# Optimization experiments

Hardware: AMD Instinct MI355X
Metric: run time of the kernel (lower is better)

The kernel has to match this reference:

```python
import jax, jax.numpy as jnp
import numpy as np

RADII = (0.8, 1.6)
NSAMPLES = (16, 32)
NUM_GRIDPOINTS = 216


def rotate_z(points, theta):
    # points (b, n, m, 3), theta (b, n); rotate xy about z-axis
    c = jnp.cos(theta)[:, :, None]
    s = jnp.sin(theta)[:, :, None]
    x, y, z = points[..., 0], points[..., 1], points[..., 2]
    return jnp.stack([c * x - s * y, s * x + c * y, z], axis=-1)


def ball_query(d2, radius, nsample):
    # d2: (b, Ng, K) squared distances. Returns first nsample in-radius point
    # indices per query (CUDA ball_query semantics: pad with first found index,
    # 0 if none found).
    K = d2.shape[-1]
    ar = jnp.arange(K, dtype=jnp.int32)
    scores = jnp.where(d2 < radius * radius, ar, K)  # K == sentinel for 'not in ball'
    idx = -jax.lax.top_k(-scores, nsample)[0]        # nsample smallest => first hits, ascending
    first = idx[..., :1]
    idx = jnp.where(idx >= K, first, idx)
    idx = jnp.where(idx >= K, 0, idx)
    return idx


def gather_group(xyz, feats_t, new_xyz, idx):
    # xyz (b,K,3), feats_t (b,K,C), new_xyz (b,Ng,3), idx (b,Ng,ns)
    gx = jax.vmap(lambda p, i: p[i])(xyz, idx)      # (b,Ng,ns,3)
    gf = jax.vmap(lambda f, i: f[i])(feats_t, idx)  # (b,Ng,ns,C)
    rel = gx - new_xyz[:, :, None, :]               # use_xyz=True relative coords
    return jnp.concatenate([rel, gf], axis=-1)      # (b,Ng,ns,3+C)


def setup_inputs() -> dict:
    key = jax.random.key(0)
    ks = jax.random.split(key, 12)
    b, n, m, K, C = 2, 48, NUM_GRIDPOINTS, 2048, 128
    proposals = jax.random.uniform(ks[0], (b, n, 7), dtype=jnp.float32)
    keypoint_xyz = jax.random.normal(ks[1], (b, K, 3), dtype=jnp.float32)
    keypoint_features = jax.random.normal(ks[2], (b, C, K), dtype=jnp.float32)
    grid_noise = jax.random.uniform(ks[3], (b, n, m, 3), dtype=jnp.float32)

    def lin(k, o, i):
        return jax.random.normal(k, (o, i), dtype=jnp.float32) / np.float32(np.sqrt(i))

    w0_0 = lin(ks[4], 64, C + 3)
    w0_1 = lin(ks[5], 64, 64)
    w1_0 = lin(ks[6], 64, C + 3)
    w1_1 = lin(ks[7], 64, 64)
    red_w0 = lin(ks[8], 256, 128 * m)
    red_w1 = lin(ks[9], 256, 256)
    z64 = jnp.zeros((64,), jnp.float32)
    return {
        'proposals': proposals, 'keypoint_xyz': keypoint_xyz,
        'keypoint_features': keypoint_features, 'grid_noise': grid_noise,
        'w0_0': w0_0, 'b0_0': z64, 'w0_1': w0_1, 'b0_1': z64,
        'w1_0': w1_0, 'b1_0': z64, 'w1_1': w1_1, 'b1_1': z64,
        'red_w0': red_w0, 'red_b0': jnp.zeros((256,), jnp.float32),
        'red_w1': red_w1, 'red_b1': jnp.zeros((256,), jnp.float32),
    }


def reference(proposals, keypoint_xyz, keypoint_features, grid_noise,
              w0_0, b0_0, w0_1, b0_1, w1_0, b1_0, w1_1, b1_1,
              red_w0, red_b0, red_w1, red_b1):
    b, n, _ = proposals.shape
    m = NUM_GRIDPOINTS
    # sample_gridpoints: uniform in box dims, rotate by yaw, shift to center
    grid = grid_noise * proposals[:, :, None, 3:6]
    grid = rotate_z(grid, proposals[..., 6]) + proposals[:, :, None, 0:3]
    new_xyz = grid.reshape(b, n * m, 3)                      # (b, Ng, 3)
    # squared pairwise distances via |a|^2 + |b|^2 - 2ab (avoids (b,Ng,K,3) temp)
    d2 = (jnp.sum(new_xyz * new_xyz, -1)[:, :, None]
          + jnp.sum(keypoint_xyz * keypoint_xyz, -1)[:, None, :]
          - 2.0 * jnp.einsum('bnd,bkd->bnk', new_xyz, keypoint_xyz))
    feats_t = jnp.transpose(keypoint_features, (0, 2, 1))    # (b, K, C)
    scale_params = [((w0_0, b0_0), (w0_1, b0_1)), ((w1_0, b1_0), (w1_1, b1_1))]
    outs = []
    for radius, ns, layers in zip(RADII, NSAMPLES, scale_params):
        idx = ball_query(d2, radius, ns)                     # (b, Ng, ns)
        x = gather_group(keypoint_xyz, feats_t, new_xyz, idx)  # (b, Ng, ns, 3+C)
        for W, bias in layers:                               # shared 1x1-conv MLP (BN folded)
            x = jax.nn.relu(jnp.einsum('bnsc,oc->bnso', x, W) + bias)
        outs.append(jnp.max(x, axis=2))                      # max-pool over neighbors
    x = jnp.concatenate(outs, axis=-1)                       # (b, Ng, Cout)
    Cout = x.shape[-1]
    # (b, Cout, n, m).permute(0,2,1,3).view(b, n, Cout*m) equivalent
    x = x.reshape(b, n, m, Cout).transpose(0, 1, 3, 2).reshape(b, n, Cout * m)
    x = jax.nn.relu(x @ red_w0.T + red_b0)
    x = jax.nn.relu(x @ red_w1.T + red_b1)
    return x
```

## Files before the change

### kernel.cpp

```cpp
#include <hip/hip_runtime.h>
#include <cstdint>

#define NPROP  48
#define MGRID  216
#define NPT    (NPROP*MGRID)
#define KPT    2048
#define CFEAT  128
#define R0SQ   0.64f
#define R1SQ   2.56f
#define NS0    16
#define NS1    32
#define KRED   (CFEAT*MGRID)
#define NPOINTS (2*NPT)
#define NKSPLIT 108

typedef float f32x4  __attribute__((ext_vector_type(4)));
typedef short bf16x8 __attribute__((ext_vector_type(8)));
typedef unsigned long long ull;

#define AFRAG_OFF 0
#define KX4_OFF   8192
#define Q0_OFF    24576
#define POOL_OFF  548864
#define PT_OFF    3203072
#define PART_OFF  5857280

__device__ __forceinline__ unsigned short bf_rne(float x) {
    unsigned u = __float_as_uint(x);
    return (unsigned short)((u + 0x7fffu + ((u >> 16) & 1u)) >> 16);
}
__device__ __forceinline__ float bf_f32(unsigned short h) {
    return __uint_as_float(((unsigned)h) << 16);
}

__global__ __launch_bounds__(64) void k_pre(
    const float* __restrict__ kxyz,
    const float* __restrict__ w01, const float* __restrict__ w11,
    float* __restrict__ ws)
{
    int bid = blockIdx.x;
    if (bid < 16) {
        int kc = bid & 1, ot = (bid >> 1) & 3, s = bid >> 3;
        const float* W = s ? w11 : w01;
        int l   = threadIdx.x;
        int row = ot*16 + (l & 15);
        int k0  = kc*32 + (l >> 4)*8;
        union { unsigned short u16[8]; bf16x8 v; } hh, hl;
#pragma unroll
        for (int j = 0; j < 8; ++j) {
            float x  = W[row*64 + k0 + j];
            unsigned short hi = bf_rne(x);
            hh.u16[j] = hi;
            hl.u16[j] = bf_rne(x - bf_f32(hi));
        }
        bf16x8* Ahi = (bf16x8*)(ws + AFRAG_OFF);
        bf16x8* Alo = Ahi + 16*64;
        int fi = (s*4 + ot)*2 + kc;
        Ahi[fi*64 + l] = hh.v;
        Alo[fi*64 + l] = hl.v;
    } else {
        int idx = (bid - 16)*64 + threadIdx.x;
        const float* kp = kxyz + (size_t)idx*3;
        float kx = kp[0], ky = kp[1], kz = kp[2];
        float kn2 = fmaf(kz, kz, fmaf(ky, ky, kx*kx));
        f32x4 v = {kx, ky, kz, kn2};
        ((f32x4*)(ws + KX4_OFF))[idx] = v;
    }
}

__global__ __launch_bounds__(256) void k_qproj(
    const float* __restrict__ kxyz, const float* __restrict__ feats,
    const float* __restrict__ w0, const float* __restrict__ b0,
    const float* __restrict__ w1, const float* __restrict__ b1,
    float* __restrict__ ws)
{
    __shared__ float wl[64*131];
    int bid  = blockIdx.x;
    int kgrp = bid & 511;
    int s    = (bid >> 9) & 1;
    int b    = bid >> 10;
    const float* W    = s ? w1 : w0;
    const float* bias = s ? b1 : b0;
    for (int i = threadIdx.x; i < 64*131; i += 256) wl[i] = W[i];
    __syncthreads();
    int k = kgrp*4 + (threadIdx.x >> 6);
    int o = threadIdx.x & 63;
    float acc = bias[o];
    const float* kp = kxyz + ((size_t)b*KPT + k)*3;
    acc = fmaf(wl[o*131+0], kp[0], acc);
    acc = fmaf(wl[o*131+1], kp[1], acc);
    acc = fmaf(wl[o*131+2], kp[2], acc);
    const float* f = feats + (size_t)b*CFEAT*KPT + k;
#pragma unroll 8
    for (int c = 0; c < CFEAT; ++c)
        acc = fmaf(wl[o*131+3+c], f[(size_t)c*KPT], acc);
    ws[Q0_OFF + (size_t)s*(2*KPT*64) + ((size_t)b*KPT + k)*64 + o] = acc;
}

template <int NST>
__device__ __forceinline__ void build_bfrag(
    const float* __restrict__ Qb, const int* __restrict__ idxl,
    const float* __restrict__ u_lds,
    bf16x8 (&Bhi)[NST][2], bf16x8 (&Blo)[NST][2], int lane)
{
    const int g = lane >> 4;
#pragma unroll
    for (int st = 0; st < NST; ++st) {
        int sp = idxl[st*16 + (lane & 15)];
        const float* qr = Qb + ((size_t)sp << 6) + g*8;
#pragma unroll
        for (int kc = 0; kc < 2; ++kc) {
            f32x4 q0 = *(const f32x4*)(qr + kc*32);
            f32x4 q1 = *(const f32x4*)(qr + kc*32 + 4);
            f32x4 u0 = *(const f32x4*)(u_lds + kc*32 + g*8);
            f32x4 u1 = *(const f32x4*)(u_lds + kc*32 + g*8 + 4);
            union { unsigned short u16[8]; bf16x8 v; } hh, hl;
#pragma unroll
            for (int j = 0; j < 4; ++j) {
                float x = fmaxf(q0[j] - u0[j], 0.f);
                unsigned short hi = bf_rne(x);
                hh.u16[j] = hi;
                hl.u16[j] = bf_rne(x - bf_f32(hi));
                float y = fmaxf(q1[j] - u1[j], 0.f);
                unsigned short hi2 = bf_rne(y);
                hh.u16[j+4] = hi2;
                hl.u16[j+4] = bf_rne(y - bf_f32(hi2));
            }
            Bhi[st][kc] = hh.v;
            Blo[st][kc] = hl.v;
        }
    }
}

template <int NST>
__device__ __forceinline__ void mfma_eval(
    const bf16x8* __restrict__ Ahi, const bf16x8* __restrict__ Alo,
    const float* __restrict__ bs,
    const bf16x8 (&Bhi)[NST][2], const bf16x8 (&Blo)[NST][2],
    float* __restrict__ stage, int sbase, int lane)
{
    const int g = lane >> 4;
#pragma unroll
    for (int ot = 0; ot < 4; ++ot) {
        int fi = (sbase + ot)*2;
        bf16x8 ah0 = Ahi[(fi+0)*64 + lane];
        bf16x8 ah1 = Ahi[(fi+1)*64 + lane];
        bf16x8 al0 = Alo[(fi+0)*64 + lane];
        bf16x8 al1 = Alo[(fi+1)*64 + lane];
        f32x4 bv = *(const f32x4*)(bs + ot*16 + g*4);
        f32x4 rmax = {0.f, 0.f, 0.f, 0.f};
#pragma unroll
        for (int st = 0; st < NST; ++st) {
            f32x4 acc = {0.f, 0.f, 0.f, 0.f};
            acc = __builtin_amdgcn_mfma_f32_16x16x32_bf16(al0, Bhi[st][0], acc, 0,0,0);
            acc = __builtin_amdgcn_mfma_f32_16x16x32_bf16(al1, Bhi[st][1], acc, 0,0,0);
            acc = __builtin_amdgcn_mfma_f32_16x16x32_bf16(ah0, Blo[st][0], acc, 0,0,0);
            acc = __builtin_amdgcn_mfma_f32_16x16x32_bf16(ah1, Blo[st][1], acc, 0,0,0);
            acc = __builtin_amdgcn_mfma_f32_16x16x32_bf16(ah0, Bhi[st][0], acc, 0,0,0);
            acc = __builtin_amdgcn_mfma_f32_16x16x32_bf16(ah1, Bhi[st][1], acc, 0,0,0);
#pragma unroll
            for (int r = 0; r < 4; ++r)
                rmax[r] = fmaxf(rmax[r], fmaxf(acc[r] + bv[r], 0.f));
        }
#pragma unroll
        for (int m = 1; m < 16; m <<= 1) {
#pragma unroll
            for (int r = 0; r < 4; ++r)
                rmax[r] = fmaxf(rmax[r], __shfl_xor(rmax[r], m));
        }
        if ((lane & 15) == 0)
            *(f32x4*)(stage + ot*16 + g*4) = rmax;
    }
}

__global__ __launch_bounds__(256) void k_main(
    const float* __restrict__ proposals, const float* __restrict__ grid_noise,
    const float* __restrict__ w00, const float* __restrict__ b01,
    const float* __restrict__ w10, const float* __restrict__ b11,
    float* __restrict__ ws)
{
    __shared__ int idx0s[4][NS0];
    __shared__ int idx1s[4][NS1];
    __shared__ __align__(16) float u0l[4][64], u1l[4][64];
    __shared__ __align__(16) float stage[4][64];
    const int wid  = threadIdx.x >> 6;
    const int lane = threadIdx.x & 63;

    const int p = blockIdx.x*4 + wid;
    int b   = p / NPT;
    int rem = p - b*NPT;
    int i   = rem / MGRID;
    int g   = rem - i*MGRID;

    float a0x = w00[lane*131+0], a0y = w00[lane*131+1], a0z = w00[lane*131+2];
    float a1x = w10[lane*131+0], a1y = w10[lane*131+1], a1z = w10[lane*131+2];

    const float* pr = proposals  + ((size_t)b*NPROP + i)*7;
    const float* gn = grid_noise + (((size_t)b*NPROP + i)*MGRID + g)*3;
    float gx = gn[0]*pr[3], gy = gn[1]*pr[4], gz = gn[2]*pr[5];
    float th = pr[6];
    float ss = sinf(th), cc = cosf(th);
    float nx = cc*gx - ss*gy + pr[0];
    float ny = ss*gx + cc*gy + pr[1];
    float nz = gz + pr[2];
    float pn2 = nx*nx + ny*ny + nz*nz;
    u0l[wid][lane] = a0x*nx + a0y*ny + a0z*nz;
    u1l[wid][lane] = a1x*nx + a1y*ny + a1z*nz;

    int* idx0 = idx0s[wid];
    int* idx1 = idx1s[wid];
    int cnt0 = 0, cnt1 = 0;
    const f32x4* kx4 = (const f32x4*)(ws + KX4_OFF) + (size_t)b*KPT;
    ull ltm = (1ull << lane) - 1ull;

#define BQ_PROC(M, KK, CNT, IDX, NSV)                                         \
    if (M) {                                                                  \
        int pre = __popcll((M) & ltm);                                        \
        if ((((M) >> lane) & 1ull) && CNT + pre < NSV) IDX[CNT + pre] = (KK); \
        CNT += __popcll(M);                                                   \
    }

    for (int ck = 0; ck < KPT/64; ck += 2) {
        f32x4 ka = kx4[ck*64 + lane];
        f32x4 kc2 = kx4[ck*64 + 64 + lane];
        float dta = fmaf(nz, ka.z, fmaf(ny, ka.y, nx*ka.x));
        float d2a = fmaf(-2.f, dta, pn2 + ka.w);
        float dtb = fmaf(nz, kc2.z, fmaf(ny, kc2.y, nx*kc2.x));
        float d2b = fmaf(-2.f, dtb, pn2 + kc2.w);
        ull m0a = __ballot(d2a < R0SQ);
        ull m1a = __ballot(d2a < R1SQ);
        ull m0b = __ballot(d2b < R0SQ);
        ull m1b = __ballot(d2b < R1SQ);
        int kka = ck*64 + lane, kkb = kka + 64;
        BQ_PROC(m0a, kka, cnt0, idx0, NS0)
        BQ_PROC(m0b, kkb, cnt0, idx0, NS0)
        BQ_PROC(m1a, kka, cnt1, idx1, NS1)
        BQ_PROC(m1b, kkb, cnt1, idx1, NS1)
        if (cnt0 >= NS0 && cnt1 >= NS1) break;
    }
#undef BQ_PROC

    if (lane == 0) {
        if (cnt0 == 0) idx0[0] = 0;
        if (cnt1 == 0) idx1[0] = 0;
    }
    asm volatile("s_waitcnt lgkmcnt(0)" ::: "memory");
    __builtin_amdgcn_wave_barrier();
    int na0 = cnt0 ? min(cnt0, NS0) : 1;
    int na1 = cnt1 ? min(cnt1, NS1) : 1;
    int f0 = idx0[0], f1 = idx1[0];
    if (lane >= na0 && lane < NS0) idx0[lane] = f0;
    if (lane >= na1 && lane < NS1) idx1[lane] = f1;
    asm volatile("s_waitcnt lgkmcnt(0)" ::: "memory");
    __builtin_amdgcn_wave_barrier();

    const float*  Qb0 = ws + Q0_OFF + (size_t)b*(KPT*64);
    const float*  Qb1 = ws + Q0_OFF + (size_t)(2*KPT*64) + (size_t)b*(KPT*64);
    const bf16x8* Ahi = (const bf16x8*)(ws + AFRAG_OFF);
    const bf16x8* Alo = Ahi + 16*64;

    bf16x8 B0hi[1][2], B0lo[1][2], B1hi[2][2], B1lo[2][2];
    build_bfrag<1>(Qb0, idx0, u0l[wid], B0hi, B0lo, lane);
    build_bfrag<2>(Qb1, idx1, u1l[wid], B1hi, B1lo, lane);

    mfma_eval<1>(Ahi, Alo, b01, B0hi, B0lo, stage[wid], 0, lane);
    asm volatile("s_waitcnt lgkmcnt(0)" ::: "memory");
    __builtin_amdgcn_wave_barrier();
    float mx0 = stage[wid][lane];
    __builtin_amdgcn_wave_barrier();

    mfma_eval<2>(Ahi, Alo, b11, B1hi, B1lo, stage[wid], 4, lane);
    asm volatile("s_waitcnt lgkmcnt(0)" ::: "memory");
    __builtin_amdgcn_wave_barrier();
    float mx1 = stage[wid][lane];

    ws[POOL_OFF + (size_t)p*CFEAT + lane]      = mx0;
    ws[POOL_OFF + (size_t)p*CFEAT + 64 + lane] = mx1;
}

template <int W>
__device__ __forceinline__ void ptr_tile(const float* __restrict__ in,
                                         float* __restrict__ out,
                                         float* __restrict__ t, int g0)
{
    for (int idx = threadIdx.x; idx < 128*W; idx += 256) {
        int gg = idx >> 7, c = idx & 127;
        t[c*(W+1) + gg] = in[(size_t)(g0+gg)*128 + c];
    }
    __syncthreads();
    for (int idx = threadIdx.x; idx < 128*W; idx += 256) {
        int c = idx / W, gg = idx - c*W;
        out[c*216 + g0 + gg] = t[c*(W+1) + gg];
    }
}

__global__ __launch_bounds__(256) void k_ptr(float* __restrict__ ws)
{
    __shared__ float t[128*33];
    int bid = blockIdx.x;
    int row = bid / 7, tt = bid - row*7;
    const float* in = ws + POOL_OFF + (size_t)row*MGRID*CFEAT;
    float* out = ws + PT_OFF + (size_t)row*KRED;
    if (tt < 6) ptr_tile<32>(in, out, t, tt*32);
    else        ptr_tile<24>(in, out, t, 192);
}

__global__ __launch_bounds__(256) void k_red0(
    const float* __restrict__ A, const float* __restrict__ w0,
    float* __restrict__ part)
{
    __shared__ __align__(16) float Al[96*68];
    __shared__ __align__(16) float Bl[128*68];
    int bid = blockIdx.x;
    int ot  = bid & 1;
    int ks  = bid >> 1;
    int tid = threadIdx.x;
    int tx  = tid & 15, ty = tid >> 4;
    float acc[6][8] = {};

    for (int chunk = 0; chunk < 4; ++chunk) {
        int kk0 = ks*256 + chunk*64;
#pragma unroll
        for (int j = 0; j < 6; ++j) {
            int f4i = tid + j*256;
            int rr = f4i >> 4, c4 = f4i & 15;
            float4 v = *(const float4*)(A + (size_t)rr*KRED + kk0 + c4*4);
            *(float4*)(Al + rr*68 + c4*4) = v;
        }
#pragma unroll
        for (int j = 0; j < 8; ++j) {
            int f4i = tid + j*256;
            int rr = f4i >> 4, c4 = f4i & 15;
            float4 v = *(const float4*)(w0 + (size_t)(ot*128+rr)*KRED + kk0 + c4*4);
            *(float4*)(Bl + rr*68 + c4*4) = v;
        }
        __syncthreads();
#pragma unroll
        for (int k4 = 0; k4 < 16; ++k4) {
            float4 av[6], bv[8];
#pragma unroll
            for (int q = 0; q < 6; ++q) av[q] = *(const float4*)(Al + (ty*6+q)*68 + k4*4);
#pragma unroll
            for (int u = 0; u < 8; ++u) bv[u] = *(const float4*)(Bl + (u*16+tx)*68 + k4*4);
#pragma unroll
            for (int q = 0; q < 6; ++q)
#pragma unroll
                for (int u = 0; u < 8; ++u) {
                    acc[q][u] = fmaf(av[q].x, bv[u].x, acc[q][u]);
                    acc[q][u] = fmaf(av[q].y, bv[u].y, acc[q][u]);
                    acc[q][u] = fmaf(av[q].z, bv[u].z, acc[q][u]);
                    acc[q][u] = fmaf(av[q].w, bv[u].w, acc[q][u]);
                }
        }
        __syncthreads();
    }
    float* pp = part + (size_t)ks*(96*256);
#pragma unroll
    for (int q = 0; q < 6; ++q)
#pragma unroll
        for (int u = 0; u < 8; ++u)
            pp[(size_t)(ty*6+q)*256 + ot*128 + u*16 + tx] = acc[q][u];
}

__global__ __launch_bounds__(256) void k_fin(
    const float* __restrict__ part, const float* __restrict__ rb0,
    const float* __restrict__ w1, const float* __restrict__ rb1,
    float* __restrict__ out)
{
    __shared__ __align__(16) float hbuf[256];
    int r = blockIdx.x, o = threadIdx.x;
    const float* pp = part + (size_t)r*256 + o;
    float s0 = 0.f, s1 = 0.f, s2 = 0.f, s3 = 0.f;
#pragma unroll 4
    for (int ks = 0; ks < NKSPLIT; ks += 4) {
        s0 += pp[(size_t)(ks+0)*(96*256)];
        s1 += pp[(size_t)(ks+1)*(96*256)];
        s2 += pp[(size_t)(ks+2)*(96*256)];
        s3 += pp[(size_t)(ks+3)*(96*256)];
    }
    float h = fmaxf(((s0 + s1) + (s2 + s3)) + rb0[o], 0.f);
    hbuf[o] = h;
    __syncthreads();
    float a0 = rb1[o], a1 = 0.f, a2 = 0.f, a3 = 0.f;
    const float4* wrow = (const float4*)(w1 + (size_t)o*256);
    const float4* hv   = (const float4*)hbuf;
#pragma unroll 8
    for (int j = 0; j < 64; ++j) {
        float4 w = wrow[j], x = hv[j];
        a0 = fmaf(w.x, x.x, a0);
        a1 = fmaf(w.y, x.y, a1);
        a2 = fmaf(w.z, x.z, a2);
        a3 = fmaf(w.w, x.w, a3);
    }
    out[(size_t)r*256 + o] = fmaxf((a0 + a1) + (a2 + a3), 0.f);
}

extern "C" void kernel_launch(void* const* d_in, const int* in_sizes, int n_in,
                              void* d_out, int out_size, void* d_ws, size_t ws_size,
                              hipStream_t stream)
{
    (void)in_sizes; (void)n_in; (void)out_size; (void)ws_size;
    const float* proposals = (const float*)d_in[0];
    const float* kxyz      = (const float*)d_in[1];
    const float* feats     = (const float*)d_in[2];
    const float* gnoise    = (const float*)d_in[3];
    const float* w0_0 = (const float*)d_in[4];
    const float* b0_0 = (const float*)d_in[5];
    const float* w0_1 = (const float*)d_in[6];
    const float* b0_1 = (const float*)d_in[7];
    const float* w1_0 = (const float*)d_in[8];
    const float* b1_0 = (const float*)d_in[9];
    const float* w1_1 = (const float*)d_in[10];
    const float* b1_1 = (const float*)d_in[11];
    const float* rw0  = (const float*)d_in[12];
    const float* rb0  = (const float*)d_in[13];
    const float* rw1  = (const float*)d_in[14];
    const float* rb1  = (const float*)d_in[15];
    float* ws  = (float*)d_ws;
    float* out = (float*)d_out;

    k_pre  <<<  80,  64, 0, stream>>>(kxyz, w0_1, w1_1, ws);
    k_qproj<<<2048, 256, 0, stream>>>(kxyz, feats, w0_0, b0_0, w1_0, b1_0, ws);
    k_main <<<5184, 256, 0, stream>>>(proposals, gnoise,
                                      w0_0, b0_1, w1_0, b1_1, ws);
    k_ptr  <<< 672, 256, 0, stream>>>(ws);
    k_red0 <<< 216, 256, 0, stream>>>(ws + PT_OFF, rw0, ws + PART_OFF);
    k_fin  <<<  96, 256, 0, stream>>>(ws + PART_OFF, rb0, rw1, rb1, out);
}
```

Before: 259.0 us.

## Stage MFMA A-fragments in LDS, skip saturated ballots, split red0 output

k_main now copies the 32KB of precomputed bf16 A-fragments from global memory into shared memory once per block and reads the MFMA operands from LDS. The ball-query loop skips the ballot for a radius once that radius's neighbor list is full. k_red0 splits the output dimension into four 64-wide tiles instead of two 128-wide tiles, doubling the grid to 432 blocks so more CUs are busy. The costs are a 32KB shared-memory footprint per k_main block, which may cut occupancy, plus an extra block-wide sync and copy, and reloading the A tile twice as often in k_red0.

```diff
diff --git a/kernel.cpp b/kernel.cpp
--- a/kernel.cpp
+++ b/kernel.cpp
@@ -134,10 +134,10 @@
 
 template <int NST>
 __device__ __forceinline__ void mfma_eval(
-    const bf16x8* __restrict__ Ahi, const bf16x8* __restrict__ Alo,
+    const bf16x8* Ahi, const bf16x8* Alo,
     const float* __restrict__ bs,
     const bf16x8 (&Bhi)[NST][2], const bf16x8 (&Blo)[NST][2],
-    float* __restrict__ stage, int sbase, int lane)
+    float* stage, int sbase, int lane)
 {
     const int g = lane >> 4;
 #pragma unroll
@@ -179,12 +179,20 @@
     const float* __restrict__ w10, const float* __restrict__ b11,
     float* __restrict__ ws)
 {
+    __shared__ __align__(16) float afrag[8192];
     __shared__ int idx0s[4][NS0];
     __shared__ int idx1s[4][NS1];
     __shared__ __align__(16) float u0l[4][64], u1l[4][64];
     __shared__ __align__(16) float stage[4][64];
     const int wid  = threadIdx.x >> 6;
     const int lane = threadIdx.x & 63;
+
+    {
+        const f32x4* src = (const f32x4*)(ws + AFRAG_OFF);
+        f32x4* dst = (f32x4*)afrag;
+        for (int t = threadIdx.x; t < 2048; t += 256) dst[t] = src[t];
+    }
+    __syncthreads();
 
     const int p = blockIdx.x*4 + wid;
     int b   = p / NPT;
@@ -213,29 +221,32 @@
     const f32x4* kx4 = (const f32x4*)(ws + KX4_OFF) + (size_t)b*KPT;
     ull ltm = (1ull << lane) - 1ull;
 
-#define BQ_PROC(M, KK, CNT, IDX, NSV)                                         \
-    if (M) {                                                                  \
-        int pre = __popcll((M) & ltm);                                        \
-        if ((((M) >> lane) & 1ull) && CNT + pre < NSV) IDX[CNT + pre] = (KK); \
-        CNT += __popcll(M);                                                   \
+#define BQ_PROC(D2, RSQ, KK, CNT, IDX, NSV)                                   \
+    {                                                                         \
+        ull m = __ballot((D2) < RSQ);                                         \
+        if (m) {                                                              \
+            int pre = __popcll(m & ltm);                                      \
+            if (((m >> lane) & 1ull) && CNT + pre < NSV) IDX[CNT + pre] = (KK);\
+            CNT += __popcll(m);                                               \
+        }                                                                     \
     }
 
     for (int ck = 0; ck < KPT/64; ck += 2) {
-        f32x4 ka = kx4[ck*64 + lane];
+        f32x4 ka  = kx4[ck*64 + lane];
         f32x4 kc2 = kx4[ck*64 + 64 + lane];
         float dta = fmaf(nz, ka.z, fmaf(ny, ka.y, nx*ka.x));
         float d2a = fmaf(-2.f, dta, pn2 + ka.w);
         float dtb = fmaf(nz, kc2.z, fmaf(ny, kc2.y, nx*kc2.x));
         float d2b = fmaf(-2.f, dtb, pn2 + kc2.w);
-        ull m0a = __ballot(d2a < R0SQ);
-        ull m1a = __ballot(d2a < R1SQ);
-        ull m0b = __ballot(d2b < R0SQ);
-        ull m1b = __ballot(d2b < R1SQ);
         int kka = ck*64 + lane, kkb = kka + 64;
-        BQ_PROC(m0a, kka, cnt0, idx0, NS0)
-        BQ_PROC(m0b, kkb, cnt0, idx0, NS0)
-        BQ_PROC(m1a, kka, cnt1, idx1, NS1)
-        BQ_PROC(m1b, kkb, cnt1, idx1, NS1)
+        if (cnt0 < NS0) {
+            BQ_PROC(d2a, R0SQ, kka, cnt0, idx0, NS0)
+            BQ_PROC(d2b, R0SQ, kkb, cnt0, idx0, NS0)
+        }
+        if (cnt1 < NS1) {
+            BQ_PROC(d2a, R1SQ, kka, cnt1, idx1, NS1)
+            BQ_PROC(d2b, R1SQ, kkb, cnt1, idx1, NS1)
+        }
         if (cnt0 >= NS0 && cnt1 >= NS1) break;
     }
 #undef BQ_PROC
@@ -256,7 +267,7 @@
 
     const float*  Qb0 = ws + Q0_OFF + (size_t)b*(KPT*64);
     const float*  Qb1 = ws + Q0_OFF + (size_t)(2*KPT*64) + (size_t)b*(KPT*64);
-    const bf16x8* Ahi = (const bf16x8*)(ws + AFRAG_OFF);
+    const bf16x8* Ahi = (const bf16x8*)afrag;
     const bf16x8* Alo = Ahi + 16*64;
 
     bf16x8 B0hi[1][2], B0lo[1][2], B1hi[2][2], B1lo[2][2];
@@ -310,13 +321,13 @@
     float* __restrict__ part)
 {
     __shared__ __align__(16) float Al[96*68];
-    __shared__ __align__(16) float Bl[128*68];
+    __shared__ __align__(16) float Bl[64*68];
     int bid = blockIdx.x;
-    int ot  = bid & 1;
-    int ks  = bid >> 1;
+    int ot  = bid & 3;
+    int ks  = bid >> 2;
     int tid = threadIdx.x;
     int tx  = tid & 15, ty = tid >> 4;
-    float acc[6][8] = {};
+    float acc[6][4] = {};
 
     for (int chunk = 0; chunk < 4; ++chunk) {
         int kk0 = ks*256 + chunk*64;
@@ -328,24 +339,24 @@
             *(float4*)(Al + rr*68 + c4*4) = v;
         }
 #pragma unroll
-        for (int j = 0; j < 8; ++j) {
+        for (int j = 0; j < 4; ++j) {
             int f4i = tid + j*256;
             int rr = f4i >> 4, c4 = f4i & 15;
-            float4 v = *(const float4*)(w0 + (size_t)(ot*128+rr)*KRED + kk0 + c4*4);
+            float4 v = *(const float4*)(w0 + (size_t)(ot*64+rr)*KRED + kk0 + c4*4);
             *(float4*)(Bl + rr*68 + c4*4) = v;
         }
         __syncthreads();
 #pragma unroll
         for (int k4 = 0; k4 < 16; ++k4) {
-            float4 av[6], bv[8];
+            float4 av[6], bv[4];
 #pragma unroll
             for (int q = 0; q < 6; ++q) av[q] = *(const float4*)(Al + (ty*6+q)*68 + k4*4);
 #pragma unroll
-            for (int u = 0; u < 8; ++u) bv[u] = *(const float4*)(Bl + (u*16+tx)*68 + k4*4);
+            for (int u = 0; u < 4; ++u) bv[u] = *(const float4*)(Bl + (u*16+tx)*68 + k4*4);
 #pragma unroll
             for (int q = 0; q < 6; ++q)
 #pragma unroll
-                for (int u = 0; u < 8; ++u) {
+                for (int u = 0; u < 4; ++u) {
                     acc[q][u] = fmaf(av[q].x, bv[u].x, acc[q][u]);
                     acc[q][u] = fmaf(av[q].y, bv[u].y, acc[q][u]);
                     acc[q][u] = fmaf(av[q].z, bv[u].z, acc[q][u]);
@@ -358,8 +369,8 @@
 #pragma unroll
     for (int q = 0; q < 6; ++q)
 #pragma unroll
-        for (int u = 0; u < 8; ++u)
-            pp[(size_t)(ty*6+q)*256 + ot*128 + u*16 + tx] = acc[q][u];
+        for (int u = 0; u < 4; ++u)
+            pp[(size_t)(ty*6+q)*256 + ot*64 + u*16 + tx] = acc[q][u];
 }
 
 __global__ __launch_bounds__(256) void k_fin(
@@ -424,6 +435,6 @@
     k_main <<<5184, 256, 0, stream>>>(proposals, gnoise,
                                       w0_0, b0_1, w1_0, b1_1, ws);
     k_ptr  <<< 672, 256, 0, stream>>>(ws);
-    k_red0 <<< 216, 256, 0, stream>>>(ws + PT_OFF, rw0, ws + PART_OFF);
+    k_red0 <<< 432, 256, 0, stream>>>(ws + PT_OFF, rw0, ws + PART_OFF);
     k_fin  <<<  96, 256, 0, stream>>>(ws + PART_OFF, rb0, rw1, rb1, out);
 }
```

After: 247.6 us. -4.4%, faster.
